# Kernel tuning notes

Measured on AMD Instinct MI355X. Metric: run time of the kernel, lower is better.

## Reference

```python
import jax, jax.numpy as jnp
import numpy as np

TAU = 32.0


def setup_inputs() -> dict:
    key = jax.random.key(0)
    k1, k2, k3, k4, k5 = jax.random.split(key, 5)
    B, IN, E, D, M = 32768, 768, 256, 9, 10
    feature = jax.random.normal(k1, (B, IN), dtype=jnp.float32)
    category = jax.random.randint(k2, (B,), 0, D)  # unused in forward math
    # nn.Linear(input_dim, emb_dim, bias=False) stores weight [emb_dim, input_dim]
    W_topic = jax.random.normal(k3, (E, IN), dtype=jnp.float32) * (1.0 / np.sqrt(IN))
    W_domain = jax.random.normal(k4, (E, IN), dtype=jnp.float32) * (1.0 / np.sqrt(IN))
    memory = jax.random.normal(k5, (D, M, E), dtype=jnp.float32)  # stacked domain memory banks
    return {"feature": feature, "category": category, "W_topic": W_topic,
            "W_domain": W_domain, "memory": memory}


def reference(feature, category, W_topic, W_domain, memory):
    # L2-normalize features along dim 1
    f = feature / jnp.linalg.norm(feature, axis=1, keepdims=True)
    topic = f @ W_topic.T      # [B, E]
    dom = f @ W_domain.T       # [B, E]
    # per-domain memory attention, batched over all D domains at once
    att = jax.nn.softmax(jnp.einsum('be,dme->bdm', topic, memory) * TAU, axis=-1)  # [B, D, M]
    sep = jnp.einsum('bdm,dme->bde', att, memory)                                   # [B, D, E]
    domain_att = jnp.einsum('bde,be->bd', sep, dom)                                 # [B, D]
    return jax.nn.softmax(domain_att * TAU, axis=1)[:, None, :]                     # [B, 1, D]
```

## Files before the change

### kernel.cpp

```cpp
#include <hip/hip_runtime.h>
#include <math.h>

typedef __attribute__((ext_vector_type(8))) short short8;
typedef __attribute__((ext_vector_type(4))) float f32x4;
typedef __attribute__((ext_vector_type(8))) unsigned short u16x8;

#define TAUF 32.0f

constexpr int B_LO_OFF = 12288;
constexpr int BUF_SZ   = 24576;
constexpr int CSTR     = 196;

__global__ __launch_bounds__(768) void precompute_pr(
    const float* __restrict__ Wt, const float* __restrict__ Wd,
    const float* __restrict__ mem, unsigned short* __restrict__ PRhi,
    unsigned short* __restrict__ PRlo) {
  int g = blockIdx.x, t = threadIdx.x;
  int r0 = g * 2;
  if (r0 >= 180) {
    PRhi[(size_t)r0 * 768 + t] = 0;
    PRlo[(size_t)r0 * 768 + t] = 0;
    PRhi[(size_t)(r0 + 1) * 768 + t] = 0;
    PRlo[(size_t)(r0 + 1) * 768 + t] = 0;
    return;
  }
  __shared__ float mlds[512];
  const float* W = (r0 >= 90) ? Wd : Wt;
  int dm0 = (r0 >= 90) ? r0 - 90 : r0;
  if (t < 512) mlds[t] = mem[(size_t)dm0 * 256 + t];
  __syncthreads();
  float a0 = 0.f, a1 = 0.f;
  #pragma unroll 8
  for (int e = 0; e < 256; ++e) {
    float w = W[(size_t)e * 768 + t];
    a0 += mlds[e] * w;
    a1 += mlds[256 + e] * w;
  }
  float xs[2] = {a0, a1};
  #pragma unroll
  for (int rr = 0; rr < 2; ++rr) {
    unsigned int bu = __float_as_uint(xs[rr]);
    unsigned short hi = (unsigned short)(bu >> 16);
    float hf = __uint_as_float(bu & 0xffff0000u);
    unsigned short lo = (unsigned short)(__float_as_uint(xs[rr] - hf) >> 16);
    PRhi[(size_t)(r0 + rr) * 768 + t] = hi;
    PRlo[(size_t)(r0 + rr) * 768 + t] = lo;
  }
}

__global__ __launch_bounds__(256, 2) void fused_mfma(
    const float* __restrict__ feat, const unsigned short* __restrict__ PRhi,
    const unsigned short* __restrict__ PRlo, float* __restrict__ out) {
  __shared__ f32x4 smemv[3136];
  __shared__ float invn[64];
  __shared__ float sarr[576];
  char* smem = (char*)smemv;

  const int t    = threadIdx.x;
  const int lane = t & 63;
  const int wid  = t >> 6;
  const int rg   = wid >> 1;
  const int cg   = wid & 1;
  const int b0   = blockIdx.x * 64;

  const float* gA0 = feat + (size_t)(b0 + rg * 32 + (lane & 15)) * 768 +
                     ((lane >> 4) << 3);
  const float* gA1 = gA0 + 16 * 768;

  const int iid  = wid * 6;
  const int bc   = lane >> 2;
  const int bsw  = (lane & 3) ^ ((bc >> 1) & 3);
  const int bsrc = bc * 1536 + bsw * 16;

  const int bfr = ((lane & 15) << 6) |
                  ((((lane >> 4) ^ (((lane & 15) >> 1) & 3)) & 3) << 4);

  f32x4 acc0[6], acc1[6];
  #pragma unroll
  for (int j = 0; j < 6; ++j) {
    acc0[j] = (f32x4){0.f, 0.f, 0.f, 0.f};
    acc1[j] = (f32x4){0.f, 0.f, 0.f, 0.f};
  }
  float ssq0 = 0.f, ssq1 = 0.f;

  auto issueB = [&](int kt, int bb) {
    #pragma unroll
    for (int u = 0; u < 6; ++u) {
      int i  = iid + u;
      int pl = i >= 12;
      int ch = pl ? i - 12 : i;
      const unsigned short* basep = pl ? PRlo : PRhi;
      const char* gg = (const char*)basep + (size_t)ch * 16 * 1536 +
                       kt * 64 + bsrc;
      char* l = smem + bb * BUF_SZ + (pl ? B_LO_OFF : 0) + ch * 1024 +
                lane * 16;
      __builtin_amdgcn_global_load_lds((const unsigned int*)gg,
                                       (unsigned int*)l, 16, 0, 0);
    }
  };

  float4 ra0a, ra0b, ra1a, ra1b;
  auto loadA = [&](int kt) {
    ra0a = *(const float4*)(gA0 + kt * 32);
    ra0b = *(const float4*)(gA0 + kt * 32 + 4);
    ra1a = *(const float4*)(gA1 + kt * 32);
    ra1b = *(const float4*)(gA1 + kt * 32 + 4);
  };

  short8 ah0, al0, ah1, al1;
  auto cvtA = [&]() {
    float x0[8] = {ra0a.x, ra0a.y, ra0a.z, ra0a.w, ra0b.x, ra0b.y, ra0b.z, ra0b.w};
    float x1[8] = {ra1a.x, ra1a.y, ra1a.z, ra1a.w, ra1b.x, ra1b.y, ra1b.z, ra1b.w};
    u16x8 h0, l0, h1, l1;
    #pragma unroll
    for (int e = 0; e < 8; ++e) {
      float x = x0[e];
      ssq0 += x * x;
      unsigned int bu = __float_as_uint(x);
      h0[e] = (unsigned short)(bu >> 16);
      l0[e] = (unsigned short)(__float_as_uint(x - __uint_as_float(bu & 0xffff0000u)) >> 16);
      float y = x1[e];
      ssq1 += y * y;
      unsigned int bv = __float_as_uint(y);
      h1[e] = (unsigned short)(bv >> 16);
      l1[e] = (unsigned short)(__float_as_uint(y - __uint_as_float(bv & 0xffff0000u)) >> 16);
    }
    ah0 = (short8)h0; al0 = (short8)l0; ah1 = (short8)h1; al1 = (short8)l1;
  };

  auto domfma = [&](int bb) {
    char* base = smem + bb * BUF_SZ;
    #pragma unroll
    for (int j = 0; j < 6; ++j) {
      int chb = (cg * 6 + j) * 1024;
      short8 bh = *(const short8*)(base + chb + bfr);
      short8 bl = *(const short8*)(base + B_LO_OFF + chb + bfr);
      acc0[j] = __builtin_amdgcn_mfma_f32_16x16x32_bf16(ah0, bh, acc0[j], 0, 0, 0);
      acc0[j] = __builtin_amdgcn_mfma_f32_16x16x32_bf16(al0, bh, acc0[j], 0, 0, 0);
      acc0[j] = __builtin_amdgcn_mfma_f32_16x16x32_bf16(ah0, bl, acc0[j], 0, 0, 0);
      acc1[j] = __builtin_amdgcn_mfma_f32_16x16x32_bf16(ah1, bh, acc1[j], 0, 0, 0);
      acc1[j] = __builtin_amdgcn_mfma_f32_16x16x32_bf16(al1, bh, acc1[j], 0, 0, 0);
      acc1[j] = __builtin_amdgcn_mfma_f32_16x16x32_bf16(ah1, bl, acc1[j], 0, 0, 0);
    }
  };

  loadA(0);
  issueB(0, 0);
  __syncthreads();

  for (int kp = 0; kp < 11; ++kp) {
    int kt = 2 * kp;
    issueB(kt + 1, 1);
    cvtA();
    loadA(kt + 1);
    domfma(0);
    __syncthreads();
    issueB(kt + 2, 0);
    cvtA();
    loadA(kt + 2);
    domfma(1);
    __syncthreads();
  }
  issueB(23, 1);
  cvtA();
  loadA(23);
  domfma(0);
  __syncthreads();
  cvtA();
  domfma(1);

  float v0 = ssq0, v1 = ssq1;
  v0 += __shfl_xor(v0, 16, 64); v0 += __shfl_xor(v0, 32, 64);
  v1 += __shfl_xor(v1, 16, 64); v1 += __shfl_xor(v1, 32, 64);
  if (cg == 0 && lane < 16) {
    invn[rg * 32 + lane]      = rsqrtf(v0);
    invn[rg * 32 + 16 + lane] = rsqrtf(v1);
  }
  __syncthreads();

  float* Clds = (float*)smem;
  #pragma unroll
  for (int rt = 0; rt < 2; ++rt) {
    int rbase = rg * 32 + rt * 16 + ((lane >> 4) << 2);
    #pragma unroll
    for (int j = 0; j < 6; ++j) {
      int col = cg * 96 + j * 16 + (lane & 15);
      f32x4 v = rt ? acc1[j] : acc0[j];
      #pragma unroll
      for (int jj = 0; jj < 4; ++jj)
        Clds[(rbase + jj) * CSTR + col] = v[jj] * invn[rbase + jj];
    }
  }
  __syncthreads();

  for (int pid = t; pid < 576; pid += 256) {
    int row = pid / 9, d = pid - row * 9;
    const float* qp = Clds + row * CSTR + d * 10;
    const float* rp = qp + 90;
    float mx = qp[0];
    #pragma unroll
    for (int m = 1; m < 10; ++m) mx = fmaxf(mx, qp[m]);
    float s = 0.f, val = 0.f;
    #pragma unroll
    for (int m = 0; m < 10; ++m) {
      float e = __expf(TAUF * (qp[m] - mx));
      s += e;
      val += e * rp[m];
    }
    sarr[pid] = val / s;
  }
  __syncthreads();

  if (t < 64) {
    float v[9];
    #pragma unroll
    for (int d = 0; d < 9; ++d) v[d] = sarr[t * 9 + d];
    float mx = v[0];
    #pragma unroll
    for (int d = 1; d < 9; ++d) mx = fmaxf(mx, v[d]);
    float s = 0.f;
    float e[9];
    #pragma unroll
    for (int d = 0; d < 9; ++d) {
      e[d] = __expf(TAUF * (v[d] - mx));
      s += e[d];
    }
    float is = 1.f / s;
    #pragma unroll
    for (int d = 0; d < 9; ++d)
      out[(size_t)(b0 + t) * 9 + d] = e[d] * is;
  }
}

extern "C" void kernel_launch(void* const* d_in, const int* in_sizes, int n_in,
                              void* d_out, int out_size, void* d_ws, size_t ws_size,
                              hipStream_t stream) {
  const float* feat = (const float*)d_in[0];
  const float* Wt  = (const float*)d_in[2];
  const float* Wd  = (const float*)d_in[3];
  const float* mem = (const float*)d_in[4];
  float* outp = (float*)d_out;

  unsigned short* PRhi = (unsigned short*)d_ws;
  unsigned short* PRlo = PRhi + 192 * 768;

  precompute_pr<<<96, 768, 0, stream>>>(Wt, Wd, mem, PRhi, PRlo);
  const int B = in_sizes[1];
  fused_mfma<<<B / 64, 256, 0, stream>>>(feat, PRhi, PRlo, outp);
}
```

Measured before the change: 68.22 us.

## Deepen A/B prefetch pipeline with explicit vmcnt waits and batch precompute rows

The main kernel now double-buffers the feature (A) registers and prefetches two K-tiles ahead. It replaces __syncthreads with raw s_barrier plus partial s_waitcnt vmcnt so that global loads stay in flight across barriers. The precompute kernel computes six projected rows per block instead of two, so each pass over W is shared by more rows and the launch uses fewer blocks. This trades higher register pressure, and a reliance on hand-counted vmcnt values being correct, for less load latency exposed in the main loop.

```diff
diff --git a/kernel.cpp b/kernel.cpp
--- a/kernel.cpp
+++ b/kernel.cpp
@@ -15,34 +15,33 @@
     const float* __restrict__ Wt, const float* __restrict__ Wd,
     const float* __restrict__ mem, unsigned short* __restrict__ PRhi,
     unsigned short* __restrict__ PRlo) {
-  int g = blockIdx.x, t = threadIdx.x;
-  int r0 = g * 2;
+  int r0 = blockIdx.x * 6, t = threadIdx.x;
   if (r0 >= 180) {
-    PRhi[(size_t)r0 * 768 + t] = 0;
-    PRlo[(size_t)r0 * 768 + t] = 0;
-    PRhi[(size_t)(r0 + 1) * 768 + t] = 0;
-    PRlo[(size_t)(r0 + 1) * 768 + t] = 0;
+    #pragma unroll
+    for (int rr = 0; rr < 6; ++rr) {
+      PRhi[(size_t)(r0 + rr) * 768 + t] = 0;
+      PRlo[(size_t)(r0 + rr) * 768 + t] = 0;
+    }
     return;
   }
-  __shared__ float mlds[512];
+  __shared__ float mlds[1536];
   const float* W = (r0 >= 90) ? Wd : Wt;
   int dm0 = (r0 >= 90) ? r0 - 90 : r0;
-  if (t < 512) mlds[t] = mem[(size_t)dm0 * 256 + t];
-  __syncthreads();
-  float a0 = 0.f, a1 = 0.f;
-  #pragma unroll 8
+  for (int i = t; i < 1536; i += 768) mlds[i] = mem[(size_t)dm0 * 256 + i];
+  __syncthreads();
+  float a[6] = {0.f, 0.f, 0.f, 0.f, 0.f, 0.f};
+  #pragma unroll 4
   for (int e = 0; e < 256; ++e) {
     float w = W[(size_t)e * 768 + t];
-    a0 += mlds[e] * w;
-    a1 += mlds[256 + e] * w;
-  }
-  float xs[2] = {a0, a1};
+    #pragma unroll
+    for (int rr = 0; rr < 6; ++rr) a[rr] += mlds[rr * 256 + e] * w;
+  }
   #pragma unroll
-  for (int rr = 0; rr < 2; ++rr) {
-    unsigned int bu = __float_as_uint(xs[rr]);
+  for (int rr = 0; rr < 6; ++rr) {
+    unsigned int bu = __float_as_uint(a[rr]);
     unsigned short hi = (unsigned short)(bu >> 16);
     float hf = __uint_as_float(bu & 0xffff0000u);
-    unsigned short lo = (unsigned short)(__float_as_uint(xs[rr] - hf) >> 16);
+    unsigned short lo = (unsigned short)(__float_as_uint(a[rr] - hf) >> 16);
     PRhi[(size_t)(r0 + rr) * 768 + t] = hi;
     PRlo[(size_t)(r0 + rr) * 768 + t] = lo;
   }
@@ -99,16 +98,22 @@
     }
   };
 
-  float4 ra0a, ra0b, ra1a, ra1b;
-  auto loadA = [&](int kt) {
-    ra0a = *(const float4*)(gA0 + kt * 32);
-    ra0b = *(const float4*)(gA0 + kt * 32 + 4);
-    ra1a = *(const float4*)(gA1 + kt * 32);
-    ra1b = *(const float4*)(gA1 + kt * 32 + 4);
+  float4 Aa0, Aa1, Aa2, Aa3, Ab0, Ab1, Ab2, Ab3;
+  auto loadAa = [&](int kt) {
+    Aa0 = *(const float4*)(gA0 + kt * 32);
+    Aa1 = *(const float4*)(gA0 + kt * 32 + 4);
+    Aa2 = *(const float4*)(gA1 + kt * 32);
+    Aa3 = *(const float4*)(gA1 + kt * 32 + 4);
+  };
+  auto loadAb = [&](int kt) {
+    Ab0 = *(const float4*)(gA0 + kt * 32);
+    Ab1 = *(const float4*)(gA0 + kt * 32 + 4);
+    Ab2 = *(const float4*)(gA1 + kt * 32);
+    Ab3 = *(const float4*)(gA1 + kt * 32 + 4);
   };
 
   short8 ah0, al0, ah1, al1;
-  auto cvtA = [&]() {
+  auto cvtCore = [&](float4 ra0a, float4 ra0b, float4 ra1a, float4 ra1b) {
     float x0[8] = {ra0a.x, ra0a.y, ra0a.z, ra0a.w, ra0b.x, ra0b.y, ra0b.z, ra0b.w};
     float x1[8] = {ra1a.x, ra1a.y, ra1a.z, ra1a.w, ra1b.x, ra1b.y, ra1b.z, ra1b.w};
     u16x8 h0, l0, h1, l1;
@@ -144,29 +149,43 @@
     }
   };
 
-  loadA(0);
   issueB(0, 0);
-  __syncthreads();
+  issueB(1, 1);
+  loadAa(0);
+  loadAb(1);
+  asm volatile("s_waitcnt vmcnt(14)" ::: "memory");
+  __builtin_amdgcn_sched_barrier(0);
+  __builtin_amdgcn_s_barrier();
 
   for (int kp = 0; kp < 11; ++kp) {
     int kt = 2 * kp;
-    issueB(kt + 1, 1);
-    cvtA();
-    loadA(kt + 1);
+    cvtCore(Aa0, Aa1, Aa2, Aa3);
     domfma(0);
-    __syncthreads();
+    __builtin_amdgcn_sched_barrier(0);
+    __builtin_amdgcn_s_barrier();
     issueB(kt + 2, 0);
-    cvtA();
-    loadA(kt + 2);
+    loadAa(kt + 2);
+    asm volatile("s_waitcnt vmcnt(14)" ::: "memory");
+    __builtin_amdgcn_sched_barrier(0);
+    __builtin_amdgcn_s_barrier();
+    cvtCore(Ab0, Ab1, Ab2, Ab3);
     domfma(1);
-    __syncthreads();
-  }
-  issueB(23, 1);
-  cvtA();
-  loadA(23);
+    __builtin_amdgcn_sched_barrier(0);
+    __builtin_amdgcn_s_barrier();
+    issueB(kt + 3, 1);
+    loadAb(kt + 3);
+    asm volatile("s_waitcnt vmcnt(14)" ::: "memory");
+    __builtin_amdgcn_sched_barrier(0);
+    __builtin_amdgcn_s_barrier();
+  }
+  cvtCore(Aa0, Aa1, Aa2, Aa3);
   domfma(0);
-  __syncthreads();
-  cvtA();
+  __builtin_amdgcn_sched_barrier(0);
+  __builtin_amdgcn_s_barrier();
+  asm volatile("s_waitcnt vmcnt(0)" ::: "memory");
+  __builtin_amdgcn_sched_barrier(0);
+  __builtin_amdgcn_s_barrier();
+  cvtCore(Ab0, Ab1, Ab2, Ab3);
   domfma(1);
 
   float v0 = ssq0, v1 = ssq1;
@@ -244,7 +263,7 @@
   unsigned short* PRhi = (unsigned short*)d_ws;
   unsigned short* PRlo = PRhi + 192 * 768;
 
-  precompute_pr<<<96, 768, 0, stream>>>(Wt, Wd, mem, PRhi, PRlo);
+  precompute_pr<<<32, 768, 0, stream>>>(Wt, Wd, mem, PRhi, PRlo);
   const int B = in_sizes[1];
   fused_mfma<<<B / 64, 256, 0, stream>>>(feat, PRhi, PRlo, outp);
 }
```

New measurement: 74.27 us. +8.9%, slower.
